# Optimization experiments

Measured on AMD Instinct MI355X. Metric: run time of the kernel, lower is better.

The kernel has to match this reference:

```python
import jax, jax.numpy as jnp
import numpy as np
from jax import lax

EPS = 1e-06
PAD = 1


def setup_inputs() -> dict:
    key = jax.random.key(0)
    k1, k2, k3, k4, k5 = jax.random.split(key, 5)
    B, C, H, W = 16, 512, 64, 64  # in_channels == out_channels (required by the module's broadcast)
    w_dim, ksz = 512, 3
    x = jax.random.normal(k1, (B, C, H, W), dtype=jnp.float32)
    w = jax.random.normal(k2, (B, w_dim), dtype=jnp.float32)
    conv_weight = jax.random.normal(k3, (C, C, ksz, ksz), dtype=jnp.float32)
    # nn.Linear(w_dim, out_channels): weight (out, in), bias (out), default uniform init
    bound = 1.0 / np.sqrt(w_dim)
    linear_w = jax.random.uniform(k4, (C, w_dim), minval=-bound, maxval=bound, dtype=jnp.float32)
    linear_b = jax.random.uniform(k5, (C,), minval=-bound, maxval=bound, dtype=jnp.float32)
    return {"x": x, "w": w, "conv_weight": conv_weight, "linear_w": linear_w, "linear_b": linear_b}


def reference(x, w, conv_weight, linear_w, linear_b):
    B, Cin, H, W = x.shape
    # style_scale = Linear(w): (B, out_channels)
    style = jnp.einsum('bd,od->bo', w, linear_w) + linear_b
    # modulate: (1, out, in, k, k) * (B, 1, out, 1, 1)  [requires in == out, as in the source]
    w_prime = conv_weight[None] * style[:, None, :, None, None]
    # demodulate over (in, kh, kw)
    denom = jnp.sqrt(jnp.sum(w_prime ** 2, axis=(2, 3, 4), keepdims=True) + EPS)
    w_pp = w_prime / denom  # (B, out, in, k, k)
    Cout = w_pp.shape[2]
    ksz = w_pp.shape[3]
    # grouped conv trick: fold batch into channels, groups = B
    eff_x = x.reshape(1, B * Cin, H, W)
    eff_f = w_pp.reshape(B * Cout, Cin, ksz, ksz)
    out = lax.conv_general_dilated(
        eff_x, eff_f,
        window_strides=(1, 1),
        padding=[(PAD, PAD), (PAD, PAD)],
        dimension_numbers=('NCHW', 'OIHW', 'NCHW'),
        feature_group_count=B,
    )
    return out.reshape(B, Cout, H, W)
```

## Files before the change

### kernel.cpp

```cpp
#include <hip/hip_runtime.h>

typedef unsigned short ushort_t;
typedef unsigned int uint_t;
typedef __bf16 bf16x8 __attribute__((ext_vector_type(8)));
typedef float float4v __attribute__((ext_vector_type(4)));
typedef uint_t uint4v __attribute__((ext_vector_type(4)));

#define EPS 1e-6f

#define WS_STYLE   0
#define WS_INVD    32768
#define WS_WSQ     65536
#define WS_AW      1114112
#define WS_XP      6291456

__device__ __forceinline__ ushort_t f2bf(float v) {
    union { float f; uint_t u; } c; c.f = v;
    uint_t u = c.u;
    u += 0x7fffu + ((u >> 16) & 1u);
    return (ushort_t)(u >> 16);
}

__device__ __forceinline__ void gload_lds16(const void* g, void* l) {
    __builtin_amdgcn_global_load_lds(
        (const __attribute__((address_space(1))) uint_t*)g,
        (__attribute__((address_space(3))) uint_t*)l, 16, 0, 0);
}

__global__ void prep_fused1(const float* __restrict__ w, const float* __restrict__ lw,
                            const float* __restrict__ lb, const float* __restrict__ cw,
                            float* __restrict__ style, ushort_t* __restrict__ Aw,
                            float* __restrict__ wsq) {
    int blk = blockIdx.x;
    if (blk < 2048) {
        int gw = blk * 4 + (threadIdx.x >> 6);
        int lane = threadIdx.x & 63;
        int b = gw >> 9, o = gw & 511;
        float s = 0.f;
#pragma unroll
        for (int j = 0; j < 8; ++j) {
            int d = j * 64 + lane;
            s += w[b * 512 + d] * lw[o * 512 + d];
        }
#pragma unroll
        for (int off = 32; off; off >>= 1) s += __shfl_down(s, off);
        if (lane == 0) style[gw] = s + lb[o];
    } else {
        int id = (blk - 2048) * 256 + threadIdx.x;
        int o = id >> 9, i = id & 511;
        const float* p = cw + (size_t)id * 9;
        size_t base = (size_t)o * 4608 + (size_t)(i >> 6) * 576 + (i & 63);
        float s = 0.f;
#pragma unroll
        for (int t = 0; t < 9; ++t) {
            float v = p[t];
            s += v * v;
            Aw[base + t * 64] = f2bf(v);
        }
        wsq[id] = s;
    }
}

__global__ void prep_fused2(const float* __restrict__ wsq, const float* __restrict__ style,
                            float* __restrict__ invd, const float* __restrict__ x,
                            ushort_t* __restrict__ Xp) {
    __shared__ ushort_t tile[64][65];
    int blk = blockIdx.x;
    if (blk < 2048) {
        int gw = blk * 4 + (threadIdx.x >> 6);
        int lane = threadIdx.x & 63;
        int b = gw >> 9, o = gw & 511;
        float s = 0.f;
#pragma unroll
        for (int j = 0; j < 8; ++j) {
            int d = j * 64 + lane;
            float st = style[b * 512 + d];
            s += wsq[o * 512 + d] * st * st;
        }
#pragma unroll
        for (int off = 32; off; off >>= 1) s += __shfl_down(s, off);
        if (lane == 0) invd[gw] = rsqrtf(s + EPS);
    } else if (blk < 3088) {
        int j = (blk - 2048) * 4 + (threadIdx.x >> 6);
        int lane = threadIdx.x & 63;
        int b = j / 260, bp = j - b * 260;
        int py, px;
        if (bp < 66)       { py = 0;        px = bp; }
        else if (bp < 132) { py = 65;       px = bp - 66; }
        else if (bp < 196) { py = bp - 131; px = 0; }
        else               { py = bp - 195; px = 65; }
        size_t pix = ((size_t)b * 66 + py) * 66 + px;
        ((uint4v*)(Xp + pix * 512))[lane] = (uint4v){0, 0, 0, 0};
    } else {
        int mb = blk - 3088;
        int y = mb & 63;
        int chunk = mb >> 6;
        int i0 = (chunk & 7) * 64;
        int b = chunk >> 3;
        int tid = threadIdx.x;
        int sub = tid >> 6;
        int lane = tid & 63;
#pragma unroll
        for (int pass = 0; pass < 16; ++pass) {
            int ir = pass * 4 + sub;
            float s = style[b * 512 + i0 + ir];
            float v = x[(((size_t)b * 512 + i0 + ir) * 64 + y) * 64 + lane] * s;
            tile[ir][lane] = f2bf(v);
        }
        __syncthreads();
        size_t rowbase = ((size_t)b * 66 + (y + 1)) * 66 + 1;
#pragma unroll
        for (int pass = 0; pass < 2; ++pass) {
            int idx = pass * 256 + tid;
            int xx = idx >> 3;
            int ch8 = idx & 7;
            ushort_t v[8];
#pragma unroll
            for (int j = 0; j < 8; ++j) v[j] = tile[ch8 * 8 + j][xx];
            *(uint4v*)(Xp + (rowbase + xx) * 512 + i0 + ch8 * 8) = *(uint4v*)v;
        }
    }
}

__global__ __launch_bounds__(512, 2) void conv_gemm(const ushort_t* __restrict__ Aw,
                                                    const ushort_t* __restrict__ Xp,
                                                    const float* __restrict__ invd,
                                                    float* __restrict__ out) {
    __shared__ ushort_t lds[2][32768];

    const int tid  = threadIdx.x;
    const int lane = tid & 63;
    const int wv   = tid >> 6;
    const int wm   = wv >> 2;
    const int wn   = wv & 3;
    const int l15  = lane & 15;
    const int quad = lane >> 4;

    const int bid = blockIdx.x;
    const int xcd = bid & 7;
    const int ci  = bid >> 3;
    const int b   = xcd * 2 + (ci >> 5);
    const int ot  = (ci >> 4) & 1;
    const int pxt = ci & 15;
    const int o0  = ot * 256;
    const int p0  = pxt * 256;

    const int tr  = tid >> 3;
    const int gsw = (((tid & 7) ^ (tr & 7)) << 4);
    const char* Ab = (const char*)Aw;
    const char* Xb = (const char*)Xp;
    const char* aga[4];
    const char* bga[4];
#pragma unroll
    for (int s = 0; s < 4; ++s) {
        int row = s * 64 + tr;
        aga[s] = Ab + (size_t)(o0 + row) * 9216 + gsw;
        int py0 = pxt * 4 + s;
        bga[s] = Xb + ((size_t)(b * 66 + py0) * 66 + tr) * 1024 + gsw;
    }
    const int lds_wv = wv * 1024;

    const int sw0 = ((quad ^ (l15 & 7)) << 4);
    const int sw1 = (((4 + quad) ^ (l15 & 7)) << 4);
    const int aoffs = (wm * 128 + l15) * 128;
    const int boffs = 32768 + (wn * 64 + l15) * 128;

    float4v acc[8][4] = {};

    auto stage = [&](int kt) {
        const int parity = kt & 1;
        const long aoff = (long)kt * 128;
        const int iblk = (kt * 7282) >> 16;
        const int t = kt - iblk * 9;
        const int dh = t / 3, dw = t - dh * 3;
        const long boff = (long)(dh * 66 + dw) * 1024 + (long)iblk * 128;
        char* la = (char*)&lds[parity][0]     + lds_wv;
        char* lb = (char*)&lds[parity][16384] + lds_wv;
#pragma unroll
        for (int s = 0; s < 4; ++s) {
            gload_lds16(aga[s] + aoff, la + s * 8192);
            gload_lds16(bga[s] + boff, lb + s * 8192);
        }
    };

    stage(0);
    stage(1);

#pragma unroll 1
    for (int kt = 0; kt < 72; ++kt) {
        if (kt < 71) { asm volatile("s_waitcnt vmcnt(8)" ::: "memory"); }
        else         { asm volatile("s_waitcnt vmcnt(0)" ::: "memory"); }
        __builtin_amdgcn_s_barrier();

        const char* base = (const char*)&lds[kt & 1][0];
        bf16x8 a0[8], a1[8], b0[4], b1[4];
#pragma unroll
        for (int mi = 0; mi < 8; ++mi)
            a0[mi] = *(const bf16x8*)(base + aoffs + mi * 2048 + sw0);
#pragma unroll
        for (int ni = 0; ni < 4; ++ni)
            b0[ni] = *(const bf16x8*)(base + boffs + ni * 2048 + sw0);

        __builtin_amdgcn_s_setprio(1);
#pragma unroll
        for (int mi = 0; mi < 8; ++mi)
#pragma unroll
            for (int ni = 0; ni < 4; ++ni)
                acc[mi][ni] = __builtin_amdgcn_mfma_f32_16x16x32_bf16(a0[mi], b0[ni], acc[mi][ni], 0, 0, 0);
        __builtin_amdgcn_s_setprio(0);

#pragma unroll
        for (int mi = 0; mi < 8; ++mi)
            a1[mi] = *(const bf16x8*)(base + aoffs + mi * 2048 + sw1);
#pragma unroll
        for (int ni = 0; ni < 4; ++ni)
            b1[ni] = *(const bf16x8*)(base + boffs + ni * 2048 + sw1);

        asm volatile("s_waitcnt lgkmcnt(0)" ::: "memory");
        __builtin_amdgcn_s_barrier();

        if (kt < 70) stage(kt + 2);

        __builtin_amdgcn_s_setprio(1);
#pragma unroll
        for (int mi = 0; mi < 8; ++mi)
#pragma unroll
            for (int ni = 0; ni < 4; ++ni)
                acc[mi][ni] = __builtin_amdgcn_mfma_f32_16x16x32_bf16(a1[mi], b1[ni], acc[mi][ni], 0, 0, 0);
        __builtin_amdgcn_s_setprio(0);
    }

    const float* invb = invd + b * 512 + o0 + wm * 128;
    float* outb = out + ((size_t)b * 512 + o0 + wm * 128) * 4096 + p0 + wn * 64;
#pragma unroll
    for (int mi = 0; mi < 8; ++mi) {
#pragma unroll
        for (int r = 0; r < 4; ++r) {
            int m = mi * 16 + quad * 4 + r;
            float d = invb[m];
#pragma unroll
            for (int ni = 0; ni < 4; ++ni) {
                int n = ni * 16 + l15;
                outb[(size_t)m * 4096 + n] = acc[mi][ni][r] * d;
            }
        }
    }
}

extern "C" void kernel_launch(void* const* d_in, const int* in_sizes, int n_in,
                              void* d_out, int out_size, void* d_ws, size_t ws_size,
                              hipStream_t stream) {
    const float* x  = (const float*)d_in[0];
    const float* w  = (const float*)d_in[1];
    const float* cw = (const float*)d_in[2];
    const float* lw = (const float*)d_in[3];
    const float* lb = (const float*)d_in[4];
    float* out = (float*)d_out;

    char* ws = (char*)d_ws;
    float*    style = (float*)(ws + WS_STYLE);
    float*    invd  = (float*)(ws + WS_INVD);
    float*    wsq   = (float*)(ws + WS_WSQ);
    ushort_t* Aw    = (ushort_t*)(ws + WS_AW);
    ushort_t* Xp    = (ushort_t*)(ws + WS_XP);

    prep_fused1<<<3072, 256, 0, stream>>>(w, lw, lb, cw, style, Aw, wsq);
    prep_fused2<<<11280, 256, 0, stream>>>(wsq, style, invd, x, Xp);
    conv_gemm<<<512, 512, 0, stream>>>(Aw, Xp, invd, out);
}
```

Baseline: 481.6 us.

## Software-pipeline LDS fragment reads across K-steps and vectorize x prep loads

The GEMM main loop is restructured so the first-half A/B fragments for the next K-step are read from LDS before the second-half MFMAs, and the second-half fragments are read before the first-half MFMAs. This overlaps LDS reads with MFMA work and removes one barrier per iteration. The cost is a full vmcnt(0) wait each iteration, which may reduce how far global-to-LDS prefetch can overlap. Separately, the x-prep transposes now use float4 global loads with 8-byte LDS writes, and per-stage pointer arrays are replaced by constant offsets to save registers.

```diff
diff --git a/kernel.cpp b/kernel.cpp
--- a/kernel.cpp
+++ b/kernel.cpp
@@ -5,6 +5,7 @@
 typedef __bf16 bf16x8 __attribute__((ext_vector_type(8)));
 typedef float float4v __attribute__((ext_vector_type(4)));
 typedef uint_t uint4v __attribute__((ext_vector_type(4)));
+typedef uint_t uint2v __attribute__((ext_vector_type(2)));
 
 #define EPS 1e-6f
 
@@ -64,7 +65,7 @@
 __global__ void prep_fused2(const float* __restrict__ wsq, const float* __restrict__ style,
                             float* __restrict__ invd, const float* __restrict__ x,
                             ushort_t* __restrict__ Xp) {
-    __shared__ ushort_t tile[64][65];
+    __shared__ ushort_t tile[64][66];
     int blk = blockIdx.x;
     if (blk < 2048) {
         int gw = blk * 4 + (threadIdx.x >> 6);
@@ -98,14 +99,18 @@
         int i0 = (chunk & 7) * 64;
         int b = chunk >> 3;
         int tid = threadIdx.x;
-        int sub = tid >> 6;
-        int lane = tid & 63;
-#pragma unroll
-        for (int pass = 0; pass < 16; ++pass) {
-            int ir = pass * 4 + sub;
-            float s = style[b * 512 + i0 + ir];
-            float v = x[(((size_t)b * 512 + i0 + ir) * 64 + y) * 64 + lane] * s;
-            tile[ir][lane] = f2bf(v);
+        int ch = tid >> 2;
+        int xq = tid & 3;
+        float s = style[b * 512 + i0 + ch];
+        const float* xrow = x + (((size_t)b * 512 + i0 + ch) * 64 + y) * 64;
+#pragma unroll
+        for (int pass = 0; pass < 4; ++pass) {
+            int x0 = pass * 16 + xq * 4;
+            float4v v = *(const float4v*)(xrow + x0);
+            ushort_t u[4];
+#pragma unroll
+            for (int j = 0; j < 4; ++j) u[j] = f2bf(v[j] * s);
+            *(uint2v*)(&tile[ch][x0]) = *(const uint2v*)u;
         }
         __syncthreads();
         size_t rowbase = ((size_t)b * 66 + (y + 1)) * 66 + 1;
@@ -147,17 +152,8 @@
 
     const int tr  = tid >> 3;
     const int gsw = (((tid & 7) ^ (tr & 7)) << 4);
-    const char* Ab = (const char*)Aw;
-    const char* Xb = (const char*)Xp;
-    const char* aga[4];
-    const char* bga[4];
-#pragma unroll
-    for (int s = 0; s < 4; ++s) {
-        int row = s * 64 + tr;
-        aga[s] = Ab + (size_t)(o0 + row) * 9216 + gsw;
-        int py0 = pxt * 4 + s;
-        bga[s] = Xb + ((size_t)(b * 66 + py0) * 66 + tr) * 1024 + gsw;
-    }
+    const char* aga0 = (const char*)Aw + (size_t)(o0 + tr) * 9216 + gsw;
+    const char* bga0 = (const char*)Xp + ((size_t)(b * 66 + pxt * 4) * 66 + tr) * 1024 + gsw;
     const int lds_wv = wv * 1024;
 
     const int sw0 = ((quad ^ (l15 & 7)) << 4);
@@ -166,40 +162,44 @@
     const int boffs = 32768 + (wn * 64 + l15) * 128;
 
     float4v acc[8][4] = {};
-
-    auto stage = [&](int kt) {
-        const int parity = kt & 1;
-        const long aoff = (long)kt * 128;
-        const int iblk = (kt * 7282) >> 16;
-        const int t = kt - iblk * 9;
+    bf16x8 a0[8], b0[4], a1[8], b1[4];
+
+    auto stage = [&](int kt2) {
+        const int parity = kt2 & 1;
+        const long aoff = (long)kt2 * 128;
+        const int iblk = (kt2 * 7282) >> 16;
+        const int t = kt2 - iblk * 9;
         const int dh = t / 3, dw = t - dh * 3;
         const long boff = (long)(dh * 66 + dw) * 1024 + (long)iblk * 128;
         char* la = (char*)&lds[parity][0]     + lds_wv;
         char* lb = (char*)&lds[parity][16384] + lds_wv;
 #pragma unroll
         for (int s = 0; s < 4; ++s) {
-            gload_lds16(aga[s] + aoff, la + s * 8192);
-            gload_lds16(bga[s] + boff, lb + s * 8192);
+            gload_lds16(aga0 + (size_t)s * 589824 + aoff, la + s * 8192);
+            gload_lds16(bga0 + (size_t)s * 67584  + boff, lb + s * 8192);
         }
     };
 
     stage(0);
     stage(1);
+    asm volatile("s_waitcnt vmcnt(8)" ::: "memory");
+    __builtin_amdgcn_s_barrier();
+    {
+        const char* base = (const char*)&lds[0][0];
+#pragma unroll
+        for (int ni = 0; ni < 4; ++ni) b0[ni] = *(const bf16x8*)(base + boffs + ni * 2048 + sw0);
+#pragma unroll
+        for (int mi = 0; mi < 8; ++mi) a0[mi] = *(const bf16x8*)(base + aoffs + mi * 2048 + sw0);
+    }
 
 #pragma unroll 1
     for (int kt = 0; kt < 72; ++kt) {
-        if (kt < 71) { asm volatile("s_waitcnt vmcnt(8)" ::: "memory"); }
-        else         { asm volatile("s_waitcnt vmcnt(0)" ::: "memory"); }
-        __builtin_amdgcn_s_barrier();
-
-        const char* base = (const char*)&lds[kt & 1][0];
-        bf16x8 a0[8], a1[8], b0[4], b1[4];
-#pragma unroll
-        for (int mi = 0; mi < 8; ++mi)
-            a0[mi] = *(const bf16x8*)(base + aoffs + mi * 2048 + sw0);
-#pragma unroll
-        for (int ni = 0; ni < 4; ++ni)
-            b0[ni] = *(const bf16x8*)(base + boffs + ni * 2048 + sw0);
+        const char* cbase = (const char*)&lds[kt & 1][0];
+
+#pragma unroll
+        for (int ni = 0; ni < 4; ++ni) b1[ni] = *(const bf16x8*)(cbase + boffs + ni * 2048 + sw1);
+#pragma unroll
+        for (int mi = 0; mi < 8; ++mi) a1[mi] = *(const bf16x8*)(cbase + aoffs + mi * 2048 + sw1);
 
         __builtin_amdgcn_s_setprio(1);
 #pragma unroll
@@ -209,16 +209,17 @@
                 acc[mi][ni] = __builtin_amdgcn_mfma_f32_16x16x32_bf16(a0[mi], b0[ni], acc[mi][ni], 0, 0, 0);
         __builtin_amdgcn_s_setprio(0);
 
-#pragma unroll
-        for (int mi = 0; mi < 8; ++mi)
-            a1[mi] = *(const bf16x8*)(base + aoffs + mi * 2048 + sw1);
-#pragma unroll
-        for (int ni = 0; ni < 4; ++ni)
-            b1[ni] = *(const bf16x8*)(base + boffs + ni * 2048 + sw1);
-
         asm volatile("s_waitcnt lgkmcnt(0)" ::: "memory");
+        asm volatile("s_waitcnt vmcnt(0)" ::: "memory");
         __builtin_amdgcn_s_barrier();
 
+        if (kt < 71) {
+            const char* nbase = (const char*)&lds[(kt + 1) & 1][0];
+#pragma unroll
+            for (int ni = 0; ni < 4; ++ni) b0[ni] = *(const bf16x8*)(nbase + boffs + ni * 2048 + sw0);
+#pragma unroll
+            for (int mi = 0; mi < 8; ++mi) a0[mi] = *(const bf16x8*)(nbase + aoffs + mi * 2048 + sw0);
+        }
         if (kt < 70) stage(kt + 2);
 
         __builtin_amdgcn_s_setprio(1);
```

After: 471.4 us. 2.1% less time.
